# Optimization experiments

Hardware: AMD Instinct MI355X
Metric: run time of the kernel (lower is better)

## Reference

```python
import jax, jax.numpy as jnp
import numpy as np

BN_EPS = 1e-5


def setup_inputs() -> dict:
    key = jax.random.key(0)
    k_x, k_A, k_W, k_b = jax.random.split(key, 4)
    N, C_in, T, V = 32, 64, 300, 25
    P, C_out = 3, 128
    x = jax.random.normal(k_x, (N, C_in, T, V), dtype=jnp.float32)
    # adjacency partitions: nonnegative, row-normalized-ish (rand in [0,1))
    A = jax.random.uniform(k_A, (P, V, V), dtype=jnp.float32)
    # kaiming fan_in init for 1x1 conv weights: std = sqrt(2/fan_in)
    W = jax.random.normal(k_W, (P, C_out, C_in), dtype=jnp.float32) * np.sqrt(2.0 / C_in)
    b = jax.random.normal(k_b, (P, C_out), dtype=jnp.float32) * 0.01
    gamma = jnp.ones((C_out,), dtype=jnp.float32)
    beta = jnp.zeros((C_out,), dtype=jnp.float32)
    return {"x": x, "A": A, "W": W, "b": b, "gamma": gamma, "beta": beta}


def reference(x, A, W, b, gamma, beta):
    # x: (N, C, T, V); A: (P, V, V); W: (P, C_out, C_in); b: (P, C_out)
    # Per partition p: aggregate over graph (x @ A_p), then 1x1 conv, then sum over p.
    # Fused: y[n,o,t,v] = sum_p sum_c W[p,o,c] * (sum_w x[n,c,t,w] * A[p,w,v]) + sum_p b[p,o]
    xa = jnp.einsum('nctw,pwv->pnctv', x, A)            # (P, N, C_in, T, V)
    y = jnp.einsum('pnctv,poc->notv', xa, W)            # (N, C_out, T, V)
    y = y + jnp.sum(b, axis=0)[None, :, None, None]
    # BatchNorm2d, training-mode forward: stats over (N, T, V), biased variance
    mean = jnp.mean(y, axis=(0, 2, 3), keepdims=True)
    var = jnp.mean(jnp.square(y - mean), axis=(0, 2, 3), keepdims=True)
    y = (y - mean) * jax.lax.rsqrt(var + BN_EPS)
    y = y * gamma[None, :, None, None] + beta[None, :, None, None]
    return jax.nn.relu(y)
```

## Files before the change

kernel.cpp:

```cpp
#include <hip/hip_runtime.h>
#include <hip/hip_bf16.h>

#define NN 32
#define CIN 64
#define TTOT 300
#define VV 25
#define PP 3
#define COUT 128
#define KTOT 192
#define TTILE 5
#define NTILES 60
#define CNT 240000.0f
#define NCOLS 240000
#define SBLK 375

#define XSTR 40
#define ZSTR 72
#define ZROWS 128

#define WS_STATS 0
#define WS_SCALE 256
#define WS_SHIFT 384
#define WS_BSUM  512
#define WS_W2    640
#define WS_PART  32768
#define ZT_BYTE_OFF (1u << 20)
#define WS_NEEDED (ZT_BYTE_OFF + (size_t)NCOLS * KTOT * 2)

typedef float f32x4 __attribute__((ext_vector_type(4)));
typedef short s16x8 __attribute__((ext_vector_type(8)));

__device__ __forceinline__ short f2bf(float f) {
    unsigned u = __float_as_uint(f);
    u += 0x7fff + ((u >> 16) & 1);
    return (short)(u >> 16);
}

__device__ __forceinline__ void gl_lds16(const void* g, void* l) {
    __builtin_amdgcn_global_load_lds(
        (const __attribute__((address_space(1))) unsigned int*)g,
        (__attribute__((address_space(3))) unsigned int*)l, 16, 0, 0);
}

__global__ __launch_bounds__(256) void prep_kernel(const float* __restrict__ W,
                                                   const float* __restrict__ b,
                                                   float* __restrict__ ws) {
    int tid = blockIdx.x * blockDim.x + threadIdx.x;
    if (tid < 256) ws[WS_STATS + tid] = 0.0f;
    if (tid >= 256 && tid < 384) {
        int o = tid - 256;
        ws[WS_BSUM + o] = b[o] + b[COUT + o] + b[2 * COUT + o];
    }
    if (tid < COUT * KTOT) {
        int o = tid / KTOT, k = tid % KTOT;
        int p = k / 64, c = k % 64;
        ((short*)(ws + WS_W2))[tid] = f2bf(W[(p * COUT + o) * CIN + c]);
    }
}


__global__ __launch_bounds__(512, 4) void agg_kernel(const float* __restrict__ x,
                                                     const float* __restrict__ A,
                                                     short* __restrict__ Zt) {
    __shared__ __align__(16) short Xs[TTILE * 64 * XSTR];
    __shared__ __align__(16) short Ats[PP * 32 * XSTR];

    const int tid  = threadIdx.x;
    const int lane = tid & 63;
    const int wave = tid >> 6;
    const int n  = blockIdx.x / NTILES;
    const int t0 = (blockIdx.x % NTILES) * TTILE;
    const int lg = lane >> 4;
    const int li = lane & 15;

    {
        const float* xb = x + (size_t)n * (CIN * TTOT * VV) + (size_t)t0 * VV;
        #pragma unroll
        for (int it = 0; it < 20; ++it) {
            int i = tid + it * 512;
            int c = i / 160;
            int r2 = i - c * 160;
            int t = r2 >> 5, w = r2 & 31;
            float val = (w < VV) ? xb[c * (TTOT * VV) + t * VV + w] : 0.0f;
            Xs[(t * 64 + c) * XSTR + w] = f2bf(val);
        }
        #pragma unroll
        for (int it = 0; it < 8; ++it) {
            int i = tid + it * 512;
            if (i < PP * 32 * XSTR) {
                int p = i / (32 * XSTR);
                int r = i - p * (32 * XSTR);
                int v = r / XSTR, w = r - v * XSTR;
                Ats[i] = (v < VV && w < VV) ? f2bf(A[p * (VV * VV) + w * VV + v])
                                            : (short)0;
            }
        }
    }
    __syncthreads();

    const int cf = wave >> 1;
    const int vf = wave & 1;
    const int vv = vf * 16 + li;

    s16x8 xa[TTILE];
    #pragma unroll
    for (int t = 0; t < TTILE; ++t)
        xa[t] = *(const s16x8*)(&Xs[(t * 64 + cf * 16 + li) * XSTR + lg * 8]);
    s16x8 af[PP];
    #pragma unroll
    for (int p = 0; p < PP; ++p)
        af[p] = *(const s16x8*)(&Ats[(p * 32 + vf * 16 + li) * XSTR + lg * 8]);

    const bool vok = (vv < VV);
    const size_t colbase = (size_t)n * 7500 + (size_t)t0 * VV + vv;
    #pragma unroll
    for (int t = 0; t < TTILE; ++t) {
        #pragma unroll
        for (int p = 0; p < PP; ++p) {
            f32x4 z = (f32x4){0.f, 0.f, 0.f, 0.f};
            f32x4 d = __builtin_amdgcn_mfma_f32_16x16x32_bf16(xa[t], af[p], z, 0, 0, 0);
            if (vok) {
                ushort4 pk;
                pk.x = (unsigned short)f2bf(d[0]);
                pk.y = (unsigned short)f2bf(d[1]);
                pk.z = (unsigned short)f2bf(d[2]);
                pk.w = (unsigned short)f2bf(d[3]);
                *(ushort4*)(&Zt[(colbase + (size_t)t * VV) * KTOT
                                + p * 64 + cf * 16 + lg * 4]) = pk;
            }
        }
    }
}

__global__ __launch_bounds__(512, 4) void conv_stats(const short* __restrict__ Zt,
                                                     float* __restrict__ ws) {
    __shared__ __align__(16) short Zs[128 * KTOT];
    __shared__ float sstat[256];
    const int tid  = threadIdx.x;
    const int lane = tid & 63;
    const int wave = tid >> 6;
    const int lg = lane >> 4;
    const int li = lane & 15;
    const int blk = blockIdx.x;

    const short* w2 = (const short*)(ws + WS_W2);
    const float* bsum = ws + WS_BSUM;
    const int ow = wave >> 1;
    const int ch = wave & 1;
    const int o0 = ow * 32;

    s16x8 wf[2][6];
    #pragma unroll
    for (int mf = 0; mf < 2; ++mf)
        #pragma unroll
        for (int ks = 0; ks < 6; ++ks)
            wf[mf][ks] = *(const s16x8*)(w2 + (o0 + mf * 16 + li) * KTOT
                                            + ks * 32 + lg * 8);

    if (tid < 256) sstat[tid] = 0.0f;

    float s[2][4], sq[2][4];
    #pragma unroll
    for (int mf = 0; mf < 2; ++mf)
        #pragma unroll
        for (int r = 0; r < 4; ++r) { s[mf][r] = 0.f; sq[mf][r] = 0.f; }

    #pragma unroll 1
    for (int ti = 0; ti < 5; ++ti) {
        const int c0 = (blk * 5 + ti) * 128;
        {
            const char* ztb = (const char*)Zt + (size_t)c0 * 384;
            char* lb = (char*)Zs + (size_t)wave * 1024;
            #pragma unroll
            for (int it = 0; it < 6; ++it) {
                int chunk = it * 512 + tid;
                int col = chunk / 24;
                int within = (chunk - col * 24) * 16;
                int srcoff = within ^ ((col & 7) << 4);
                gl_lds16(ztb + (size_t)col * 384 + srcoff, lb + (size_t)it * 8192);
            }
        }
        __syncthreads();

        f32x4 acc[2][4];
        #pragma unroll
        for (int mf = 0; mf < 2; ++mf)
            #pragma unroll
            for (int cf = 0; cf < 4; ++cf)
                acc[mf][cf] = (f32x4){0.f, 0.f, 0.f, 0.f};

        #pragma unroll
        for (int cf = 0; cf < 4; ++cf) {
            int col = ch * 64 + cf * 16 + li;
            int rb = col * 384;
            int sw = (col & 7) << 4;
            #pragma unroll
            for (int ks = 0; ks < 6; ++ks) {
                s16x8 zf = *(const s16x8*)((const char*)Zs
                                           + ((rb + ks * 64 + lg * 16) ^ sw));
                acc[0][cf] = __builtin_amdgcn_mfma_f32_16x16x32_bf16(wf[0][ks], zf,
                                                                     acc[0][cf], 0, 0, 0);
                acc[1][cf] = __builtin_amdgcn_mfma_f32_16x16x32_bf16(wf[1][ks], zf,
                                                                     acc[1][cf], 0, 0, 0);
            }
        }

        #pragma unroll
        for (int mf = 0; mf < 2; ++mf) {
            #pragma unroll
            for (int r = 0; r < 4; ++r) {
                float bo = bsum[o0 + mf * 16 + lg * 4 + r];
                #pragma unroll
                for (int cf = 0; cf < 4; ++cf) {
                    float val = acc[mf][cf][r] + bo;
                    s[mf][r] += val;
                    sq[mf][r] += val * val;
                }
            }
        }
        __syncthreads();
    }

    #pragma unroll
    for (int mf = 0; mf < 2; ++mf) {
        #pragma unroll
        for (int r = 0; r < 4; ++r) {
            float a = s[mf][r], b = sq[mf][r];
            #pragma unroll
            for (int m = 1; m < 16; m <<= 1) {
                a += __shfl_xor(a, m, 64);
                b += __shfl_xor(b, m, 64);
            }
            if (li == 0) {
                int o = o0 + mf * 16 + lg * 4 + r;
                atomicAdd(&sstat[o], a);
                atomicAdd(&sstat[128 + o], b);
            }
        }
    }
    __syncthreads();
    if (tid < 256) ws[WS_PART + blk * 256 + tid] = sstat[tid];
}

__global__ void finalize_partials(const float* __restrict__ gamma,
                                  const float* __restrict__ beta,
                                  float* ws) {
    __shared__ float red[2];
    const int o = blockIdx.x;
    const int wave = threadIdx.x >> 6;
    const int lane = threadIdx.x & 63;
    float acc = 0.f;
    #pragma unroll
    for (int it = 0; it < 6; ++it) {
        int blk = lane + it * 64;
        if (blk < SBLK) acc += ws[WS_PART + blk * 256 + wave * 128 + o];
    }
    #pragma unroll
    for (int m = 1; m < 64; m <<= 1) acc += __shfl_xor(acc, m, 64);
    if (lane == 0) red[wave] = acc;
    __syncthreads();
    if (threadIdx.x == 0) {
        float mean = red[0] * (1.0f / CNT);
        float ex2  = red[1] * (1.0f / CNT);
        float var  = ex2 - mean * mean;
        float rstd = rsqrtf(var + 1e-5f);
        float sc = gamma[o] * rstd;
        ws[WS_SCALE + o] = sc;
        ws[WS_SHIFT + o] = beta[o] - mean * sc;
    }
}

__global__ __launch_bounds__(512, 4) void conv_apply(const short* __restrict__ Zt,
                                                     float* __restrict__ y,
                                                     const float* __restrict__ ws) {
    __shared__ __align__(16) short Zs[128 * KTOT];
    const int tid  = threadIdx.x;
    const int lane = tid & 63;
    const int wave = tid >> 6;
    const int lg = lane >> 4;
    const int li = lane & 15;
    const int c0 = blockIdx.x * 128;

    {
        const char* ztb = (const char*)Zt + (size_t)c0 * 384;
        char* lb = (char*)Zs + (size_t)wave * 1024;
        #pragma unroll
        for (int it = 0; it < 6; ++it) {
            int chunk = it * 512 + tid;
            int col = chunk / 24;
            int within = (chunk - col * 24) * 16;
            int srcoff = within ^ ((col & 7) << 4);
            gl_lds16(ztb + (size_t)col * 384 + srcoff, lb + (size_t)it * 8192);
        }
    }

    const short* w2 = (const short*)(ws + WS_W2);
    const int ow = wave >> 1;
    const int ch = wave & 1;
    const int o0 = ow * 32;
    s16x8 wf[2][6];
    #pragma unroll
    for (int mf = 0; mf < 2; ++mf)
        #pragma unroll
        for (int ks = 0; ks < 6; ++ks)
            wf[mf][ks] = *(const s16x8*)(w2 + (o0 + mf * 16 + li) * KTOT
                                            + ks * 32 + lg * 8);

    f32x4 acc[2][4];
    #pragma unroll
    for (int mf = 0; mf < 2; ++mf)
        #pragma unroll
        for (int cf = 0; cf < 4; ++cf)
            acc[mf][cf] = (f32x4){0.f, 0.f, 0.f, 0.f};

    __syncthreads();

    #pragma unroll
    for (int cf = 0; cf < 4; ++cf) {
        int col = ch * 64 + cf * 16 + li;
        int rb = col * 384;
        int sw = (col & 7) << 4;
        #pragma unroll
        for (int ks = 0; ks < 6; ++ks) {
            s16x8 zf = *(const s16x8*)((const char*)Zs
                                       + ((rb + ks * 64 + lg * 16) ^ sw));
            acc[0][cf] = __builtin_amdgcn_mfma_f32_16x16x32_bf16(wf[0][ks], zf,
                                                                 acc[0][cf], 0, 0, 0);
            acc[1][cf] = __builtin_amdgcn_mfma_f32_16x16x32_bf16(wf[1][ks], zf,
                                                                 acc[1][cf], 0, 0, 0);
        }
    }

    const float* bsum = ws + WS_BSUM;
    const float* scale = ws + WS_SCALE;
    const float* shift = ws + WS_SHIFT;
    #pragma unroll
    for (int mf = 0; mf < 2; ++mf) {
        float4 scv = *(const float4*)(scale + o0 + mf * 16 + lg * 4);
        float4 shv = *(const float4*)(shift + o0 + mf * 16 + lg * 4);
        float4 bov = *(const float4*)(bsum  + o0 + mf * 16 + lg * 4);
        float scr[4] = {scv.x, scv.y, scv.z, scv.w};
        float shr[4] = {shv.x, shv.y, shv.z, shv.w};
        float bor[4] = {bov.x, bov.y, bov.z, bov.w};
        #pragma unroll
        for (int r = 0; r < 4; ++r) {
            int o = o0 + mf * 16 + lg * 4 + r;
            #pragma unroll
            for (int cf = 0; cf < 4; ++cf) {
                int col = c0 + ch * 64 + cf * 16 + li;
                float val = acc[mf][cf][r] + bor[r];
                val = fmaxf(val * scr[r] + shr[r], 0.0f);
                int n = col / 7500;
                int inner = col - n * 7500;
                y[(size_t)(n * COUT + o) * 7500 + inner] = val;
            }
        }
    }
}

__global__ __launch_bounds__(512, 4) void sgcn_main(const float* __restrict__ x,
                                                    const float* __restrict__ A,
                                                    float* __restrict__ y,
                                                    float* ws) {
    __shared__ __align__(16) short Xs[TTILE * 64 * XSTR];
    __shared__ __align__(16) short Ats[PP * 32 * XSTR];
    __shared__ __align__(16) short Z2s[ZROWS * ZSTR];
    __shared__ float sstat[256];

    const int tid  = threadIdx.x;
    const int lane = tid & 63;
    const int wave = tid >> 6;
    const int n  = blockIdx.x / NTILES;
    const int t0 = (blockIdx.x % NTILES) * TTILE;
    const int lg = lane >> 4;
    const int li = lane & 15;

    {
        const float* xb = x + (size_t)n * (CIN * TTOT * VV) + (size_t)t0 * VV;
        #pragma unroll
        for (int it = 0; it < 20; ++it) {
            int i = tid + it * 512;
            int c = i / 160;
            int r2 = i - c * 160;
            int t = r2 >> 5, w = r2 & 31;
            float val = (w < VV) ? xb[c * (TTOT * VV) + t * VV + w] : 0.0f;
            Xs[(t * 64 + c) * XSTR + w] = f2bf(val);
        }
        #pragma unroll
        for (int it = 0; it < 8; ++it) {
            int i = tid + it * 512;
            if (i < PP * 32 * XSTR) {
                int p = i / (32 * XSTR);
                int r = i - p * (32 * XSTR);
                int v = r / XSTR, w = r - v * XSTR;
                Ats[i] = (v < VV && w < VV) ? f2bf(A[p * (VV * VV) + w * VV + v])
                                            : (short)0;
            }
        }
        if (tid < 108) ((int*)(Z2s + 125 * ZSTR))[tid] = 0;
        if (tid < 256) sstat[tid] = 0.0f;
    }
    __syncthreads();

    const int ow = wave >> 1;
    const int cw = wave & 1;
    const int o0 = ow * 32;
    const short* w2 = (const short*)(ws + WS_W2);

    f32x4 acc[2][4];
    #pragma unroll
    for (int mf = 0; mf < 2; ++mf)
        #pragma unroll
        for (int cf = 0; cf < 4; ++cf)
            acc[mf][cf] = (f32x4){0.f, 0.f, 0.f, 0.f};

    for (int p = 0; p < PP; ++p) {
        s16x8 wfl[2][2];
        #pragma unroll
        for (int mf = 0; mf < 2; ++mf)
            #pragma unroll
            for (int ks = 0; ks < 2; ++ks)
                wfl[mf][ks] = *(const s16x8*)(w2 + (o0 + mf * 16 + li) * KTOT
                                                 + p * 64 + ks * 32 + lg * 8);
        #pragma unroll
        for (int q = 0; q < 5; ++q) {
            int f = wave * 5 + q;
            int t = f >> 3, rem = f & 7;
            int vf = rem >> 2, cfr = rem & 3;
            s16x8 af = *(const s16x8*)(&Ats[(p * 32 + vf * 16 + li) * XSTR + lg * 8]);
            s16x8 bf = *(const s16x8*)(&Xs[(t * 64 + cfr * 16 + li) * XSTR + lg * 8]);
            f32x4 z = (f32x4){0.f, 0.f, 0.f, 0.f};
            f32x4 d = __builtin_amdgcn_mfma_f32_16x16x32_bf16(af, bf, z, 0, 0, 0);
            int m0 = vf * 16 + lg * 4;
            int ccol = cfr * 16 + li;
            #pragma unroll
            for (int r = 0; r < 4; ++r) {
                int m = m0 + r;
                if (m < VV) Z2s[(t * VV + m) * ZSTR + ccol] = f2bf(d[r]);
            }
        }
        __syncthreads();
        #pragma unroll
        for (int cf = 0; cf < 4; ++cf) {
            int col0 = cw * 64 + cf * 16;
            #pragma unroll
            for (int ks = 0; ks < 2; ++ks) {
                s16x8 zf = *(const s16x8*)(&Z2s[(col0 + li) * ZSTR + ks * 32 + lg * 8]);
                #pragma unroll
                for (int mf = 0; mf < 2; ++mf)
                    acc[mf][cf] = __builtin_amdgcn_mfma_f32_16x16x32_bf16(
                        wfl[mf][ks], zf, acc[mf][cf], 0, 0, 0);
            }
        }
        __syncthreads();
    }

    const float* bsum = ws + WS_BSUM;
    #pragma unroll
    for (int mf = 0; mf < 2; ++mf) {
        #pragma unroll
        for (int r = 0; r < 4; ++r) {
            int o = o0 + mf * 16 + lg * 4 + r;
            float bo = bsum[o];
            float s = 0.f, sq = 0.f;
            #pragma unroll
            for (int cf = 0; cf < 4; ++cf) {
                int col = cw * 64 + cf * 16 + li;
                float val = acc[mf][cf][r] + bo;
                if (col < TTILE * VV) {
                    y[(size_t)(n * COUT + o) * (TTOT * VV) + t0 * VV + col] = val;
                    s += val; sq += val * val;
                }
            }
            #pragma unroll
            for (int m = 1; m < 16; m <<= 1) {
                s  += __shfl_xor(s, m, 64);
                sq += __shfl_xor(sq, m, 64);
            }
            if (li == 0) {
                atomicAdd(&sstat[o], s);
                atomicAdd(&sstat[128 + o], sq);
            }
        }
    }
    __syncthreads();
    if (tid < 256) atomicAdd(&ws[WS_STATS + tid], sstat[tid]);
}

__global__ void finalize_kernel(const float* __restrict__ gamma,
                                const float* __restrict__ beta,
                                float* ws) {
    int o = threadIdx.x;
    float mean = ws[WS_STATS + o] * (1.0f / CNT);
    float ex2  = ws[WS_STATS + 128 + o] * (1.0f / CNT);
    float var  = ex2 - mean * mean;
    float rstd = rsqrtf(var + 1e-5f);
    float sc = gamma[o] * rstd;
    ws[WS_SCALE + o] = sc;
    ws[WS_SHIFT + o] = beta[o] - mean * sc;
}

__global__ __launch_bounds__(256) void norm_relu_kernel(float* __restrict__ y,
                                                        const float* __restrict__ ws) {
    const int total8 = (NN * COUT * TTOT * VV) / 8;
    const float* scale = ws + WS_SCALE;
    const float* shift = ws + WS_SHIFT;
    for (int i = blockIdx.x * blockDim.x + threadIdx.x; i < total8;
         i += gridDim.x * blockDim.x) {
        size_t base = (size_t)i * 8;
        int row0 = (int)(base / 7500);
        int row1 = (int)((base + 7) / 7500);
        int o0 = row0 & 127, o1 = row1 & 127;
        float s0 = scale[o0], h0 = shift[o0];
        float s1 = scale[o1], h1 = shift[o1];
        size_t bnd = (size_t)(row0 + 1) * 7500;
        float4 a = *(const float4*)(y + base);
        float4 b = *(const float4*)(y + base + 4);
        float vals[8] = {a.x, a.y, a.z, a.w, b.x, b.y, b.z, b.w};
        #pragma unroll
        for (int e = 0; e < 8; ++e) {
            bool first = (base + (size_t)e) < bnd;
            float sv = first ? s0 : s1;
            float hv = first ? h0 : h1;
            vals[e] = fmaxf(vals[e] * sv + hv, 0.0f);
        }
        a = make_float4(vals[0], vals[1], vals[2], vals[3]);
        b = make_float4(vals[4], vals[5], vals[6], vals[7]);
        *(float4*)(y + base) = a;
        *(float4*)(y + base + 4) = b;
    }
}

extern "C" void kernel_launch(void* const* d_in, const int* in_sizes, int n_in,
                              void* d_out, int out_size, void* d_ws, size_t ws_size,
                              hipStream_t stream) {
    const float* x     = (const float*)d_in[0];
    const float* A     = (const float*)d_in[1];
    const float* W     = (const float*)d_in[2];
    const float* b     = (const float*)d_in[3];
    const float* gamma = (const float*)d_in[4];
    const float* beta  = (const float*)d_in[5];
    float* y  = (float*)d_out;
    float* ws = (float*)d_ws;

    prep_kernel<<<96, 256, 0, stream>>>(W, b, ws);
    if (ws_size >= WS_NEEDED) {
        short* Zt = (short*)((char*)d_ws + ZT_BYTE_OFF);
        agg_kernel<<<NN * NTILES, 512, 0, stream>>>(x, A, Zt);
        conv_stats<<<SBLK, 512, 0, stream>>>(Zt, ws);
        finalize_partials<<<COUT, 128, 0, stream>>>(gamma, beta, ws);
        conv_apply<<<NCOLS / 128, 512, 0, stream>>>(Zt, y, ws);
    } else {
        sgcn_main<<<NN * NTILES, 512, 0, stream>>>(x, A, y, ws);
        finalize_kernel<<<1, 128, 0, stream>>>(gamma, beta, ws);
        norm_relu_kernel<<<2048, 256, 0, stream>>>(y, ws);
    }
}
```

Baseline: 171.7 us.

## Fuse graph aggregation with conv statistics pass and read Zt directly in apply

Merges the aggregation kernel and the conv-stats kernel into one: each block writes its aggregated tile to global Zt and also into swizzled shared memory, then runs the 1x1-conv MFMA on the local tile to accumulate BN partial sums. This removes the separate pass that re-read all of Zt just for statistics. The partial-stats buffer grows to 1920 blocks, so the Zt offset moves and finalize loops over more partials. conv_apply now loads Z fragments straight from global memory instead of staging them through LDS. The fused kernel tile has only 125 valid columns out of 128, so it zero-pads the tail and masks those columns out of the statistics.

New measurement: 181.1 us. +5.4%, slower.

```diff
diff --git a/kernel.cpp b/kernel.cpp
--- a/kernel.cpp
+++ b/kernel.cpp
@@ -12,7 +12,7 @@
 #define NTILES 60
 #define CNT 240000.0f
 #define NCOLS 240000
-#define SBLK 375
+#define NBLK 1920
 
 #define XSTR 40
 #define ZSTR 72
@@ -24,7 +24,7 @@
 #define WS_BSUM  512
 #define WS_W2    640
 #define WS_PART  32768
-#define ZT_BYTE_OFF (1u << 20)
+#define ZT_BYTE_OFF (4u << 20)
 #define WS_NEEDED (ZT_BYTE_OFF + (size_t)NCOLS * KTOT * 2)
 
 typedef float f32x4 __attribute__((ext_vector_type(4)));
@@ -34,12 +34,6 @@
     unsigned u = __float_as_uint(f);
     u += 0x7fff + ((u >> 16) & 1);
     return (short)(u >> 16);
-}
-
-__device__ __forceinline__ void gl_lds16(const void* g, void* l) {
-    __builtin_amdgcn_global_load_lds(
-        (const __attribute__((address_space(1))) unsigned int*)g,
-        (__attribute__((address_space(3))) unsigned int*)l, 16, 0, 0);
 }
 
 __global__ __launch_bounds__(256) void prep_kernel(const float* __restrict__ W,
@@ -59,11 +53,14 @@
 }
 
 
-__global__ __launch_bounds__(512, 4) void agg_kernel(const float* __restrict__ x,
-                                                     const float* __restrict__ A,
-                                                     short* __restrict__ Zt) {
-    __shared__ __align__(16) short Xs[TTILE * 64 * XSTR];
-    __shared__ __align__(16) short Ats[PP * 32 * XSTR];
+__global__ __launch_bounds__(512, 4) void aggstats_kernel(const float* __restrict__ x,
+                                                          const float* __restrict__ A,
+                                                          short* __restrict__ Zt,
+                                                          float* __restrict__ ws) {
+    __shared__ __align__(16) short SM[128 * KTOT];
+    __shared__ float sstat[256];
+    short* Xs  = SM;
+    short* Ats = SM + 12800;
 
     const int tid  = threadIdx.x;
     const int lane = tid & 63;
@@ -95,24 +92,27 @@
                                             : (short)0;
             }
         }
-    }
-    __syncthreads();
-
-    const int cf = wave >> 1;
-    const int vf = wave & 1;
-    const int vv = vf * 16 + li;
-
+        if (tid < 288) ((int*)(SM + 125 * KTOT))[tid] = 0;
+        if (tid < 256) sstat[tid] = 0.0f;
+    }
+    __syncthreads();
+
+    const int acf = wave >> 1;
+    const int avf = wave & 1;
+    const int vv  = avf * 16 + li;
     s16x8 xa[TTILE];
     #pragma unroll
     for (int t = 0; t < TTILE; ++t)
-        xa[t] = *(const s16x8*)(&Xs[(t * 64 + cf * 16 + li) * XSTR + lg * 8]);
+        xa[t] = *(const s16x8*)(&Xs[(t * 64 + acf * 16 + li) * XSTR + lg * 8]);
     s16x8 af[PP];
     #pragma unroll
     for (int p = 0; p < PP; ++p)
-        af[p] = *(const s16x8*)(&Ats[(p * 32 + vf * 16 + li) * XSTR + lg * 8]);
+        af[p] = *(const s16x8*)(&Ats[(p * 32 + avf * 16 + li) * XSTR + lg * 8]);
+    __syncthreads();
 
     const bool vok = (vv < VV);
     const size_t colbase = (size_t)n * 7500 + (size_t)t0 * VV + vv;
+    const int kbase = acf * 16 + lg * 4;
     #pragma unroll
     for (int t = 0; t < TTILE; ++t) {
         #pragma unroll
@@ -125,121 +125,68 @@
                 pk.y = (unsigned short)f2bf(d[1]);
                 pk.z = (unsigned short)f2bf(d[2]);
                 pk.w = (unsigned short)f2bf(d[3]);
-                *(ushort4*)(&Zt[(colbase + (size_t)t * VV) * KTOT
-                                + p * 64 + cf * 16 + lg * 4]) = pk;
-            }
-        }
-    }
-}
-
-__global__ __launch_bounds__(512, 4) void conv_stats(const short* __restrict__ Zt,
-                                                     float* __restrict__ ws) {
-    __shared__ __align__(16) short Zs[128 * KTOT];
-    __shared__ float sstat[256];
-    const int tid  = threadIdx.x;
-    const int lane = tid & 63;
-    const int wave = tid >> 6;
-    const int lg = lane >> 4;
-    const int li = lane & 15;
-    const int blk = blockIdx.x;
+                *(ushort4*)(&Zt[(colbase + (size_t)t * VV) * KTOT + p * 64 + kbase]) = pk;
+                int lcol = t * VV + vv;
+                int byte = (lcol * 384 + (p * 64 + kbase) * 2) ^ ((lcol & 7) << 4);
+                *(ushort4*)((char*)SM + byte) = pk;
+            }
+        }
+    }
+    __syncthreads();
 
     const short* w2 = (const short*)(ws + WS_W2);
-    const float* bsum = ws + WS_BSUM;
     const int ow = wave >> 1;
     const int ch = wave & 1;
     const int o0 = ow * 32;
 
-    s16x8 wf[2][6];
+    f32x4 acc[2][4];
     #pragma unroll
     for (int mf = 0; mf < 2; ++mf)
         #pragma unroll
-        for (int ks = 0; ks < 6; ++ks)
-            wf[mf][ks] = *(const s16x8*)(w2 + (o0 + mf * 16 + li) * KTOT
-                                            + ks * 32 + lg * 8);
-
-    if (tid < 256) sstat[tid] = 0.0f;
-
-    float s[2][4], sq[2][4];
-    #pragma unroll
-    for (int mf = 0; mf < 2; ++mf)
-        #pragma unroll
-        for (int r = 0; r < 4; ++r) { s[mf][r] = 0.f; sq[mf][r] = 0.f; }
-
-    #pragma unroll 1
-    for (int ti = 0; ti < 5; ++ti) {
-        const int c0 = (blk * 5 + ti) * 128;
-        {
-            const char* ztb = (const char*)Zt + (size_t)c0 * 384;
-            char* lb = (char*)Zs + (size_t)wave * 1024;
-            #pragma unroll
-            for (int it = 0; it < 6; ++it) {
-                int chunk = it * 512 + tid;
-                int col = chunk / 24;
-                int within = (chunk - col * 24) * 16;
-                int srcoff = within ^ ((col & 7) << 4);
-                gl_lds16(ztb + (size_t)col * 384 + srcoff, lb + (size_t)it * 8192);
-            }
-        }
-        __syncthreads();
-
-        f32x4 acc[2][4];
-        #pragma unroll
-        for (int mf = 0; mf < 2; ++mf)
-            #pragma unroll
-            for (int cf = 0; cf < 4; ++cf)
-                acc[mf][cf] = (f32x4){0.f, 0.f, 0.f, 0.f};
-
+        for (int cf = 0; cf < 4; ++cf)
+            acc[mf][cf] = (f32x4){0.f, 0.f, 0.f, 0.f};
+
+    #pragma unroll
+    for (int ks = 0; ks < 6; ++ks) {
+        s16x8 wf0 = *(const s16x8*)(w2 + (o0 + li) * KTOT + ks * 32 + lg * 8);
+        s16x8 wf1 = *(const s16x8*)(w2 + (o0 + 16 + li) * KTOT + ks * 32 + lg * 8);
         #pragma unroll
         for (int cf = 0; cf < 4; ++cf) {
-            int col = ch * 64 + cf * 16 + li;
-            int rb = col * 384;
-            int sw = (col & 7) << 4;
-            #pragma unroll
-            for (int ks = 0; ks < 6; ++ks) {
-                s16x8 zf = *(const s16x8*)((const char*)Zs
-                                           + ((rb + ks * 64 + lg * 16) ^ sw));
-                acc[0][cf] = __builtin_amdgcn_mfma_f32_16x16x32_bf16(wf[0][ks], zf,
-                                                                     acc[0][cf], 0, 0, 0);
-                acc[1][cf] = __builtin_amdgcn_mfma_f32_16x16x32_bf16(wf[1][ks], zf,
-                                                                     acc[1][cf], 0, 0, 0);
-            }
-        }
-
-        #pragma unroll
-        for (int mf = 0; mf < 2; ++mf) {
-            #pragma unroll
-            for (int r = 0; r < 4; ++r) {
-                float bo = bsum[o0 + mf * 16 + lg * 4 + r];
-                #pragma unroll
-                for (int cf = 0; cf < 4; ++cf) {
-                    float val = acc[mf][cf][r] + bo;
-                    s[mf][r] += val;
-                    sq[mf][r] += val * val;
-                }
-            }
-        }
-        __syncthreads();
-    }
-
+            int lcol = ch * 64 + cf * 16 + li;
+            int byte = (lcol * 384 + ks * 64 + lg * 16) ^ ((lcol & 7) << 4);
+            s16x8 zf = *(const s16x8*)((const char*)SM + byte);
+            acc[0][cf] = __builtin_amdgcn_mfma_f32_16x16x32_bf16(wf0, zf, acc[0][cf], 0, 0, 0);
+            acc[1][cf] = __builtin_amdgcn_mfma_f32_16x16x32_bf16(wf1, zf, acc[1][cf], 0, 0, 0);
+        }
+    }
+
+    const float* bsum = ws + WS_BSUM;
     #pragma unroll
     for (int mf = 0; mf < 2; ++mf) {
         #pragma unroll
         for (int r = 0; r < 4; ++r) {
-            float a = s[mf][r], b = sq[mf][r];
+            float bo = bsum[o0 + mf * 16 + lg * 4 + r];
+            float s = 0.f, sq = 0.f;
+            #pragma unroll
+            for (int cf = 0; cf < 4; ++cf) {
+                int lcol = ch * 64 + cf * 16 + li;
+                float val = acc[mf][cf][r] + bo;
+                if (lcol < TTILE * VV) { s += val; sq += val * val; }
+            }
             #pragma unroll
             for (int m = 1; m < 16; m <<= 1) {
-                a += __shfl_xor(a, m, 64);
-                b += __shfl_xor(b, m, 64);
+                s  += __shfl_xor(s, m, 64);
+                sq += __shfl_xor(sq, m, 64);
             }
             if (li == 0) {
                 int o = o0 + mf * 16 + lg * 4 + r;
-                atomicAdd(&sstat[o], a);
-                atomicAdd(&sstat[128 + o], b);
-            }
-        }
-    }
-    __syncthreads();
-    if (tid < 256) ws[WS_PART + blk * 256 + tid] = sstat[tid];
+                atomicAdd(&sstat[o], s);
+                atomicAdd(&sstat[128 + o], sq);
+            }
+        }
+    }
+    __syncthreads();
+    if (tid < 256) ws[WS_PART + blockIdx.x * 256 + tid] = sstat[tid];
 }
 
 __global__ void finalize_partials(const float* __restrict__ gamma,
@@ -251,9 +198,9 @@
     const int lane = threadIdx.x & 63;
     float acc = 0.f;
     #pragma unroll
-    for (int it = 0; it < 6; ++it) {
+    for (int it = 0; it < NBLK / 64; ++it) {
         int blk = lane + it * 64;
-        if (blk < SBLK) acc += ws[WS_PART + blk * 256 + wave * 128 + o];
+        acc += ws[WS_PART + blk * 256 + wave * 128 + o];
     }
     #pragma unroll
     for (int m = 1; m < 64; m <<= 1) acc += __shfl_xor(acc, m, 64);
@@ -273,31 +220,17 @@
 __global__ __launch_bounds__(512, 4) void conv_apply(const short* __restrict__ Zt,
                                                      float* __restrict__ y,
                                                      const float* __restrict__ ws) {
-    __shared__ __align__(16) short Zs[128 * KTOT];
     const int tid  = threadIdx.x;
     const int lane = tid & 63;
     const int wave = tid >> 6;
     const int lg = lane >> 4;
     const int li = lane & 15;
     const int c0 = blockIdx.x * 128;
-
-    {
-        const char* ztb = (const char*)Zt + (size_t)c0 * 384;
-        char* lb = (char*)Zs + (size_t)wave * 1024;
-        #pragma unroll
-        for (int it = 0; it < 6; ++it) {
-            int chunk = it * 512 + tid;
-            int col = chunk / 24;
-            int within = (chunk - col * 24) * 16;
-            int srcoff = within ^ ((col & 7) << 4);
-            gl_lds16(ztb + (size_t)col * 384 + srcoff, lb + (size_t)it * 8192);
-        }
-    }
-
-    const short* w2 = (const short*)(ws + WS_W2);
     const int ow = wave >> 1;
     const int ch = wave & 1;
     const int o0 = ow * 32;
+
+    const short* w2 = (const short*)(ws + WS_W2);
     s16x8 wf[2][6];
     #pragma unroll
     for (int mf = 0; mf < 2; ++mf)
@@ -313,22 +246,27 @@
         for (int cf = 0; cf < 4; ++cf)
             acc[mf][cf] = (f32x4){0.f, 0.f, 0.f, 0.f};
 
-    __syncthreads();
-
     #pragma unroll
     for (int cf = 0; cf < 4; ++cf) {
-        int col = ch * 64 + cf * 16 + li;
-        int rb = col * 384;
-        int sw = (col & 7) << 4;
-        #pragma unroll
-        for (int ks = 0; ks < 6; ++ks) {
-            s16x8 zf = *(const s16x8*)((const char*)Zs
-                                       + ((rb + ks * 64 + lg * 16) ^ sw));
-            acc[0][cf] = __builtin_amdgcn_mfma_f32_16x16x32_bf16(wf[0][ks], zf,
-                                                                 acc[0][cf], 0, 0, 0);
-            acc[1][cf] = __builtin_amdgcn_mfma_f32_16x16x32_bf16(wf[1][ks], zf,
-                                                                 acc[1][cf], 0, 0, 0);
-        }
+        const short* zp = Zt + (size_t)(c0 + ch * 64 + cf * 16 + li) * KTOT + lg * 8;
+        s16x8 zf0 = *(const s16x8*)(zp);
+        s16x8 zf1 = *(const s16x8*)(zp + 32);
+        s16x8 zf2 = *(const s16x8*)(zp + 64);
+        s16x8 zf3 = *(const s16x8*)(zp + 96);
+        s16x8 zf4 = *(const s16x8*)(zp + 128);
+        s16x8 zf5 = *(const s16x8*)(zp + 160);
+        acc[0][cf] = __builtin_amdgcn_mfma_f32_16x16x32_bf16(wf[0][0], zf0, acc[0][cf], 0, 0, 0);
+        acc[1][cf] = __builtin_amdgcn_mfma_f32_16x16x32_bf16(wf[1][0], zf0, acc[1][cf], 0, 0, 0);
+        acc[0][cf] = __builtin_amdgcn_mfma_f32_16x16x32_bf16(wf[0][1], zf1, acc[0][cf], 0, 0, 0);
+        acc[1][cf] = __builtin_amdgcn_mfma_f32_16x16x32_bf16(wf[1][1], zf1, acc[1][cf], 0, 0, 0);
+        acc[0][cf] = __builtin_amdgcn_mfma_f32_16x16x32_bf16(wf[0][2], zf2, acc[0][cf], 0, 0, 0);
+        acc[1][cf] = __builtin_amdgcn_mfma_f32_16x16x32_bf16(wf[1][2], zf2, acc[1][cf], 0, 0, 0);
+        acc[0][cf] = __builtin_amdgcn_mfma_f32_16x16x32_bf16(wf[0][3], zf3, acc[0][cf], 0, 0, 0);
+        acc[1][cf] = __builtin_amdgcn_mfma_f32_16x16x32_bf16(wf[1][3], zf3, acc[1][cf], 0, 0, 0);
+        acc[0][cf] = __builtin_amdgcn_mfma_f32_16x16x32_bf16(wf[0][4], zf4, acc[0][cf], 0, 0, 0);
+        acc[1][cf] = __builtin_amdgcn_mfma_f32_16x16x32_bf16(wf[1][4], zf4, acc[1][cf], 0, 0, 0);
+        acc[0][cf] = __builtin_amdgcn_mfma_f32_16x16x32_bf16(wf[0][5], zf5, acc[0][cf], 0, 0, 0);
+        acc[1][cf] = __builtin_amdgcn_mfma_f32_16x16x32_bf16(wf[1][5], zf5, acc[1][cf], 0, 0, 0);
     }
 
     const float* bsum = ws + WS_BSUM;
@@ -546,8 +484,7 @@
     prep_kernel<<<96, 256, 0, stream>>>(W, b, ws);
     if (ws_size >= WS_NEEDED) {
         short* Zt = (short*)((char*)d_ws + ZT_BYTE_OFF);
-        agg_kernel<<<NN * NTILES, 512, 0, stream>>>(x, A, Zt);
-        conv_stats<<<SBLK, 512, 0, stream>>>(Zt, ws);
+        aggstats_kernel<<<NBLK, 512, 0, stream>>>(x, A, Zt, ws);
         finalize_partials<<<COUT, 128, 0, stream>>>(gamma, beta, ws);
         conv_apply<<<NCOLS / 128, 512, 0, stream>>>(Zt, y, ws);
     } else {
```
